# Kernel optimization log

Hardware: AMD Instinct MI355X
Metric: run time of the kernel (lower is better)

## Reference

```python
import jax, jax.numpy as jnp
import numpy as np

B, N, H = 1024, 4096, 32


def setup_inputs() -> dict:
    key = jax.random.key(0)
    ks = jax.random.split(key, 9)
    node_embedding = jax.random.normal(ks[0], (B, N, H), dtype=jnp.float32)
    mask = jax.random.randint(ks[1], (B, N), 0, 2).astype(jnp.float32)
    times = jax.random.uniform(ks[2], (B,), dtype=jnp.float32)
    idxc = jax.random.randint(ks[3], (B, 1), 0, N)
    # parameters
    vf = jax.random.uniform(ks[4], (1, H), dtype=jnp.float32)
    lim1 = 1.0 / np.sqrt(2 * H + 1)
    W1 = jax.random.uniform(ks[5], (H, 2 * H + 1), minval=-lim1, maxval=lim1, dtype=jnp.float32)
    b1 = jax.random.uniform(ks[6], (H,), minval=-lim1, maxval=lim1, dtype=jnp.float32)
    limh = 1.0 / np.sqrt(H)
    Wq = jax.random.uniform(ks[7], (H, H), minval=-limh, maxval=limh, dtype=jnp.float32)
    Wk = jax.random.uniform(ks[8], (H, H), minval=-limh, maxval=limh, dtype=jnp.float32)
    return {"node_embedding": node_embedding, "mask": mask, "times": times,
            "vf": vf, "W1": W1, "b1": b1, "Wq": Wq, "Wk": Wk, "idxc": idxc}


def reference(node_embedding, mask, times, vf, W1, b1, Wq, Wk, idxc):
    h = node_embedding.shape[-1]
    node_avg = jnp.mean(node_embedding, axis=1)                       # [B, H]
    # gather per-batch context node (idxc path; vf used only when idxc is None)
    f = jnp.take_along_axis(node_embedding, idxc[:, :, None], axis=1)[:, 0, :]  # [B, H]
    cat = jnp.concatenate([node_avg, f, times[:, None]], axis=1)      # [B, 2H+1]
    emb = cat @ W1.T + b1                                             # [B, H]
    q = emb @ Wq.T                                                    # [B, H]
    k = node_embedding @ Wk.T                                         # [B, N, H]
    scores = jnp.einsum('bh,bnh->bn', q, k) / jnp.sqrt(jnp.asarray(h, emb.dtype))
    scores = scores - mask * 999999999.0
    return jax.nn.softmax(scores, axis=-1)
```

## Files before the change

### kernel.cpp

```cpp
#include <hip/hip_runtime.h>
#include <math.h>

#define BB 1024
#define NN 4096
#define HH 32
#define PP 4
#define RK1 (NN / PP)

#define WS_PART 0
#define WS_QK   (BB * PP * HH)

__global__ __launch_bounds__(256) void k1_colsum(
    const float* __restrict__ ne, float* __restrict__ ws)
{
    const int blk = blockIdx.x;
    const int b   = blk >> 2;
    const int p   = blk & (PP - 1);
    const int tid = threadIdx.x;
    const int q8  = tid & 7;
    const int r   = tid >> 3;

    __shared__ float s_part[256 * 4];

    const float* base = ne + (size_t)b * (NN * HH)
                           + (size_t)(p * RK1 + r) * HH + q8 * 4;
    float a0 = 0.f, a1 = 0.f, a2 = 0.f, a3 = 0.f;
    #pragma unroll 8
    for (int i = 0; i < RK1 / 32; ++i) {
        const float4 v = *reinterpret_cast<const float4*>(base + i * (32 * HH));
        a0 += v.x; a1 += v.y; a2 += v.z; a3 += v.w;
    }
    *reinterpret_cast<float4*>(&s_part[tid * 4]) = make_float4(a0, a1, a2, a3);
    __syncthreads();

    if (tid < HH) {
        const int q = tid >> 2, j = tid & 3;
        float s = 0.f;
        #pragma unroll
        for (int rr = 0; rr < 32; ++rr) s += s_part[(rr * 8 + q) * 4 + j];
        ws[WS_PART + (b * PP + p) * HH + tid] = s;
    }
}

__global__ __launch_bounds__(64) void k2_mlp(
    const float* __restrict__ ne, const float* __restrict__ times,
    const float* __restrict__ W1, const float* __restrict__ b1,
    const float* __restrict__ Wq, const float* __restrict__ Wk,
    const int* __restrict__ idxc, float* __restrict__ ws)
{
    const int b   = blockIdx.x;
    const int tid = threadIdx.x;
    __shared__ float sh_avg[HH], sh_f[HH], sh_emb[HH], sh_q[HH];

    if (tid < HH) {
        float s = 0.f;
        #pragma unroll
        for (int p = 0; p < PP; ++p) s += ws[WS_PART + (b * PP + p) * HH + tid];
        sh_avg[tid] = s * (1.0f / (float)NN);
        sh_f[tid]   = ne[(size_t)b * (NN * HH) + (size_t)idxc[b] * HH + tid];
    }
    __syncthreads();
    if (tid < HH) {
        const float t = times[b];
        const float* w = W1 + tid * (2 * HH + 1);
        float e = b1[tid];
        #pragma unroll
        for (int j = 0; j < HH; ++j) e += sh_avg[j] * w[j];
        #pragma unroll
        for (int j = 0; j < HH; ++j) e += sh_f[j] * w[HH + j];
        e += t * w[2 * HH];
        sh_emb[tid] = e;
    }
    __syncthreads();
    if (tid < HH) {
        const float* w = Wq + tid * HH;
        float qv = 0.f;
        #pragma unroll
        for (int j = 0; j < HH; ++j) qv += sh_emb[j] * w[j];
        sh_q[tid] = qv;
    }
    __syncthreads();
    if (tid < HH) {
        float s = 0.f;
        #pragma unroll
        for (int h = 0; h < HH; ++h) s += sh_q[h] * Wk[h * HH + tid];
        ws[WS_QK + b * HH + tid] = s * 0.17677669529663687f;
    }
}

__global__ __launch_bounds__(256) void k3_scores(
    const float* __restrict__ ne, const float* __restrict__ mask,
    const float* __restrict__ ws, float* __restrict__ out)
{
    const int b   = blockIdx.x;
    const int tid = threadIdx.x;
    const int q8  = tid & 7;
    const int r   = tid >> 3;

    __shared__ float s_scores[NN];
    __shared__ float sh_qk[HH];
    __shared__ float red_buf[4];

    if (tid < HH) sh_qk[tid] = ws[WS_QK + b * HH + tid];
    __syncthreads();

    const float kq0 = sh_qk[q8 * 4 + 0];
    const float kq1 = sh_qk[q8 * 4 + 1];
    const float kq2 = sh_qk[q8 * 4 + 2];
    const float kq3 = sh_qk[q8 * 4 + 3];

    const float* base = ne + (size_t)b * (NN * HH) + (size_t)r * HH + q8 * 4;

    #pragma unroll 8
    for (int i = 0; i < NN / 32; ++i) {
        const float4 v = *reinterpret_cast<const float4*>(base + i * (32 * HH));
        float p = v.x * kq0 + v.y * kq1 + v.z * kq2 + v.w * kq3;
        p += __shfl_xor(p, 1);
        p += __shfl_xor(p, 2);
        p += __shfl_xor(p, 4);
        if (q8 == 0) s_scores[r + i * 32] = p;
    }
    __syncthreads();

    const float* mrow = mask + (size_t)b * NN;
    float lmax = -INFINITY;
    #pragma unroll
    for (int k = 0; k < NN / 256; ++k) {
        const int n = tid + k * 256;
        const float sc = s_scores[n] - mrow[n] * 999999999.0f;
        s_scores[n] = sc;
        lmax = fmaxf(lmax, sc);
    }
    #pragma unroll
    for (int m = 1; m < 64; m <<= 1) lmax = fmaxf(lmax, __shfl_xor(lmax, m));
    if ((tid & 63) == 0) red_buf[tid >> 6] = lmax;
    __syncthreads();
    const float bmax = fmaxf(fmaxf(red_buf[0], red_buf[1]),
                             fmaxf(red_buf[2], red_buf[3]));

    float lsum = 0.f;
    #pragma unroll
    for (int k = 0; k < NN / 256; ++k) {
        const int n = tid + k * 256;
        const float e = expf(s_scores[n] - bmax);
        s_scores[n] = e;
        lsum += e;
    }
    #pragma unroll
    for (int m = 1; m < 64; m <<= 1) lsum += __shfl_xor(lsum, m);
    __syncthreads();
    if ((tid & 63) == 0) red_buf[tid >> 6] = lsum;
    __syncthreads();
    const float inv = 1.0f / (red_buf[0] + red_buf[1] + red_buf[2] + red_buf[3]);

    float* orow = out + (size_t)b * NN;
    #pragma unroll
    for (int k = 0; k < NN / 256; ++k) {
        const int n = tid + k * 256;
        orow[n] = s_scores[n] * inv;
    }
}

extern "C" void kernel_launch(void* const* d_in, const int* in_sizes, int n_in,
                              void* d_out, int out_size, void* d_ws, size_t ws_size,
                              hipStream_t stream) {
    (void)in_sizes; (void)n_in; (void)ws_size; (void)out_size;
    const float* ne    = (const float*)d_in[0];
    const float* mask  = (const float*)d_in[1];
    const float* times = (const float*)d_in[2];
    const float* W1    = (const float*)d_in[4];
    const float* b1    = (const float*)d_in[5];
    const float* Wq    = (const float*)d_in[6];
    const float* Wk    = (const float*)d_in[7];
    const int*   idxc  = (const int*)d_in[8];
    float* out = (float*)d_out;
    float* ws  = (float*)d_ws;

    k1_colsum<<<dim3(BB * PP), dim3(256), 0, stream>>>(ne, ws);
    k2_mlp<<<dim3(BB), dim3(64), 0, stream>>>(ne, times, W1, b1, Wq, Wk, idxc, ws);
    k3_scores<<<dim3(BB), dim3(256), 0, stream>>>(ne, mask, ws, out);
}
```

Measured before the change: 200.6 us.

## Pipeline column-sum and score stages across batch chunks in one fused kernel

Merges the MLP step into the score kernel and splits the batch into chunks. Each launch runs the column sums for chunk c alongside the MLP and softmax for chunk c-1. Because both stages read the same batch rows close together in time, the second read of node embeddings can hit in the last-level cache instead of HBM. The cost is 9 launches instead of 3, plus a branchy fused kernel that reserves the large shared-memory allocation even in the column-sum blocks, which may lower their occupancy.

Measured after the change: 617.2 us. 208% more time.

```diff
diff --git a/kernel.cpp b/kernel.cpp
--- a/kernel.cpp
+++ b/kernel.cpp
@@ -6,51 +6,71 @@
 #define HH 32
 #define PP 4
 #define RK1 (NN / PP)
+#define CHUNK 128
+#define NCH (BB / CHUNK)
+#define K1B (CHUNK * PP)
+#define K3B CHUNK
 
 #define WS_PART 0
-#define WS_QK   (BB * PP * HH)
 
-__global__ __launch_bounds__(256) void k1_colsum(
-    const float* __restrict__ ne, float* __restrict__ ws)
+__global__ __launch_bounds__(256) void pipe(
+    const float* __restrict__ ne,
+    const float* __restrict__ mask,
+    const float* __restrict__ times,
+    const float* __restrict__ W1,
+    const float* __restrict__ b1,
+    const float* __restrict__ Wq,
+    const float* __restrict__ Wk,
+    const int*   __restrict__ idxc,
+    float* __restrict__ ws,
+    float* __restrict__ out,
+    int k1c, int k3c)
 {
-    const int blk = blockIdx.x;
-    const int b   = blk >> 2;
-    const int p   = blk & (PP - 1);
+    __shared__ float smem[NN + 160];
     const int tid = threadIdx.x;
+
+    if ((int)blockIdx.x < K1B) {
+        if (k1c < 0) return;
+        const int blk = blockIdx.x;
+        const int b   = k1c * CHUNK + (blk >> 2);
+        const int p   = blk & (PP - 1);
+        const int q8  = tid & 7;
+        const int r   = tid >> 3;
+
+        float* s_part = smem;
+
+        const float* base = ne + (size_t)b * (NN * HH)
+                               + (size_t)(p * RK1 + r) * HH + q8 * 4;
+        float a0 = 0.f, a1 = 0.f, a2 = 0.f, a3 = 0.f;
+        #pragma unroll 8
+        for (int i = 0; i < RK1 / 32; ++i) {
+            const float4 v = *reinterpret_cast<const float4*>(base + i * (32 * HH));
+            a0 += v.x; a1 += v.y; a2 += v.z; a3 += v.w;
+        }
+        *reinterpret_cast<float4*>(&s_part[tid * 4]) = make_float4(a0, a1, a2, a3);
+        __syncthreads();
+
+        if (tid < HH) {
+            const int q = tid >> 2, j = tid & 3;
+            float s = 0.f;
+            #pragma unroll
+            for (int rr = 0; rr < 32; ++rr) s += s_part[(rr * 8 + q) * 4 + j];
+            ws[WS_PART + (b * PP + p) * HH + tid] = s;
+        }
+        return;
+    }
+
+    if (k3c < 0) return;
+    const int b   = k3c * CHUNK + ((int)blockIdx.x - K1B);
     const int q8  = tid & 7;
     const int r   = tid >> 3;
 
-    __shared__ float s_part[256 * 4];
-
-    const float* base = ne + (size_t)b * (NN * HH)
-                           + (size_t)(p * RK1 + r) * HH + q8 * 4;
-    float a0 = 0.f, a1 = 0.f, a2 = 0.f, a3 = 0.f;
-    #pragma unroll 8
-    for (int i = 0; i < RK1 / 32; ++i) {
-        const float4 v = *reinterpret_cast<const float4*>(base + i * (32 * HH));
-        a0 += v.x; a1 += v.y; a2 += v.z; a3 += v.w;
-    }
-    *reinterpret_cast<float4*>(&s_part[tid * 4]) = make_float4(a0, a1, a2, a3);
-    __syncthreads();
-
-    if (tid < HH) {
-        const int q = tid >> 2, j = tid & 3;
-        float s = 0.f;
-        #pragma unroll
-        for (int rr = 0; rr < 32; ++rr) s += s_part[(rr * 8 + q) * 4 + j];
-        ws[WS_PART + (b * PP + p) * HH + tid] = s;
-    }
-}
-
-__global__ __launch_bounds__(64) void k2_mlp(
-    const float* __restrict__ ne, const float* __restrict__ times,
-    const float* __restrict__ W1, const float* __restrict__ b1,
-    const float* __restrict__ Wq, const float* __restrict__ Wk,
-    const int* __restrict__ idxc, float* __restrict__ ws)
-{
-    const int b   = blockIdx.x;
-    const int tid = threadIdx.x;
-    __shared__ float sh_avg[HH], sh_f[HH], sh_emb[HH], sh_q[HH];
+    float* s_scores = smem;
+    float* sh_avg   = smem + NN;
+    float* sh_f     = smem + NN + 32;
+    float* sh_emb   = smem + NN + 64;
+    float* sh_qk    = smem + NN + 96;
+    float* red_buf  = smem + NN + 128;
 
     if (tid < HH) {
         float s = 0.f;
@@ -77,31 +97,15 @@
         float qv = 0.f;
         #pragma unroll
         for (int j = 0; j < HH; ++j) qv += sh_emb[j] * w[j];
-        sh_q[tid] = qv;
+        sh_f[tid] = qv;
     }
     __syncthreads();
     if (tid < HH) {
         float s = 0.f;
         #pragma unroll
-        for (int h = 0; h < HH; ++h) s += sh_q[h] * Wk[h * HH + tid];
-        ws[WS_QK + b * HH + tid] = s * 0.17677669529663687f;
+        for (int h = 0; h < HH; ++h) s += sh_f[h] * Wk[h * HH + tid];
+        sh_qk[tid] = s * 0.17677669529663687f;
     }
-}
-
-__global__ __launch_bounds__(256) void k3_scores(
-    const float* __restrict__ ne, const float* __restrict__ mask,
-    const float* __restrict__ ws, float* __restrict__ out)
-{
-    const int b   = blockIdx.x;
-    const int tid = threadIdx.x;
-    const int q8  = tid & 7;
-    const int r   = tid >> 3;
-
-    __shared__ float s_scores[NN];
-    __shared__ float sh_qk[HH];
-    __shared__ float red_buf[4];
-
-    if (tid < HH) sh_qk[tid] = ws[WS_QK + b * HH + tid];
     __syncthreads();
 
     const float kq0 = sh_qk[q8 * 4 + 0];
@@ -176,7 +180,12 @@
     float* out = (float*)d_out;
     float* ws  = (float*)d_ws;
 
-    k1_colsum<<<dim3(BB * PP), dim3(256), 0, stream>>>(ne, ws);
-    k2_mlp<<<dim3(BB), dim3(64), 0, stream>>>(ne, times, W1, b1, Wq, Wk, idxc, ws);
-    k3_scores<<<dim3(BB), dim3(256), 0, stream>>>(ne, mask, ws, out);
+    pipe<<<dim3(K1B), dim3(256), 0, stream>>>(
+        ne, mask, times, W1, b1, Wq, Wk, idxc, ws, out, 0, -1);
+    for (int c = 1; c < NCH; ++c) {
+        pipe<<<dim3(K1B + K3B), dim3(256), 0, stream>>>(
+            ne, mask, times, W1, b1, Wq, Wk, idxc, ws, out, c, c - 1);
+    }
+    pipe<<<dim3(K1B + K3B), dim3(256), 0, stream>>>(
+        ne, mask, times, W1, b1, Wq, Wk, idxc, ws, out, -1, NCH - 1);
 }
```

## Split score/softmax kernel across four row chunks with two-pass rescale

Applied to the files above, without the earlier changes.

The score kernel now runs four blocks per batch row, each computing scores for a quarter of the nodes, a local max and sum, and writing unnormalized exponentials plus per-chunk stats. A new rescale kernel merges the chunk stats online-softmax style and rescales the output in place. This raises block count and parallelism for the bandwidth-heavy pass over node_embedding, but adds an extra read and write of the output and one more launch.

New measurement: 213.2 us. +6.3%, slower.

```diff
diff --git a/kernel.cpp b/kernel.cpp
--- a/kernel.cpp
+++ b/kernel.cpp
@@ -6,9 +6,12 @@
 #define HH 32
 #define PP 4
 #define RK1 (NN / PP)
+#define QQ 4
+#define RQ (NN / QQ)
 
 #define WS_PART 0
 #define WS_QK   (BB * PP * HH)
+#define WS_MS   (WS_QK + BB * HH)
 
 __global__ __launch_bounds__(256) void k1_colsum(
     const float* __restrict__ ne, float* __restrict__ ws)
@@ -88,20 +91,27 @@
     }
 }
 
-__global__ __launch_bounds__(256) void k3_scores(
+__global__ __launch_bounds__(256) void k3a_scores(
     const float* __restrict__ ne, const float* __restrict__ mask,
-    const float* __restrict__ ws, float* __restrict__ out)
-{
-    const int b   = blockIdx.x;
+    const float* __restrict__ ws, float* __restrict__ out,
+    float* __restrict__ ws_ms)
+{
+    const int blk = blockIdx.x;
+    const int b   = blk >> 2;
+    const int q   = blk & (QQ - 1);
     const int tid = threadIdx.x;
     const int q8  = tid & 7;
     const int r   = tid >> 3;
 
-    __shared__ float s_scores[NN];
+    __shared__ float s_scores[RQ];
     __shared__ float sh_qk[HH];
     __shared__ float red_buf[4];
+    __shared__ float red_sum[4];
 
     if (tid < HH) sh_qk[tid] = ws[WS_QK + b * HH + tid];
+
+    const float4 mv = *reinterpret_cast<const float4*>(
+        mask + (size_t)b * NN + q * RQ + tid * 4);
     __syncthreads();
 
     const float kq0 = sh_qk[q8 * 4 + 0];
@@ -109,10 +119,11 @@
     const float kq2 = sh_qk[q8 * 4 + 2];
     const float kq3 = sh_qk[q8 * 4 + 3];
 
-    const float* base = ne + (size_t)b * (NN * HH) + (size_t)r * HH + q8 * 4;
+    const float* base = ne + (size_t)b * (NN * HH)
+                           + (size_t)(q * RQ + r) * HH + q8 * 4;
 
     #pragma unroll 8
-    for (int i = 0; i < NN / 32; ++i) {
+    for (int i = 0; i < RQ / 32; ++i) {
         const float4 v = *reinterpret_cast<const float4*>(base + i * (32 * HH));
         float p = v.x * kq0 + v.y * kq1 + v.z * kq2 + v.w * kq3;
         p += __shfl_xor(p, 1);
@@ -122,15 +133,13 @@
     }
     __syncthreads();
 
-    const float* mrow = mask + (size_t)b * NN;
-    float lmax = -INFINITY;
-    #pragma unroll
-    for (int k = 0; k < NN / 256; ++k) {
-        const int n = tid + k * 256;
-        const float sc = s_scores[n] - mrow[n] * 999999999.0f;
-        s_scores[n] = sc;
-        lmax = fmaxf(lmax, sc);
-    }
+    const float4 s4 = *reinterpret_cast<const float4*>(&s_scores[tid * 4]);
+    float sc0 = s4.x - mv.x * 999999999.0f;
+    float sc1 = s4.y - mv.y * 999999999.0f;
+    float sc2 = s4.z - mv.z * 999999999.0f;
+    float sc3 = s4.w - mv.w * 999999999.0f;
+
+    float lmax = fmaxf(fmaxf(sc0, sc1), fmaxf(sc2, sc3));
     #pragma unroll
     for (int m = 1; m < 64; m <<= 1) lmax = fmaxf(lmax, __shfl_xor(lmax, m));
     if ((tid & 63) == 0) red_buf[tid >> 6] = lmax;
@@ -138,27 +147,49 @@
     const float bmax = fmaxf(fmaxf(red_buf[0], red_buf[1]),
                              fmaxf(red_buf[2], red_buf[3]));
 
-    float lsum = 0.f;
-    #pragma unroll
-    for (int k = 0; k < NN / 256; ++k) {
-        const int n = tid + k * 256;
-        const float e = expf(s_scores[n] - bmax);
-        s_scores[n] = e;
-        lsum += e;
-    }
+    const float e0 = expf(sc0 - bmax);
+    const float e1 = expf(sc1 - bmax);
+    const float e2 = expf(sc2 - bmax);
+    const float e3 = expf(sc3 - bmax);
+    float lsum = (e0 + e1) + (e2 + e3);
     #pragma unroll
     for (int m = 1; m < 64; m <<= 1) lsum += __shfl_xor(lsum, m);
-    __syncthreads();
-    if ((tid & 63) == 0) red_buf[tid >> 6] = lsum;
-    __syncthreads();
-    const float inv = 1.0f / (red_buf[0] + red_buf[1] + red_buf[2] + red_buf[3]);
-
-    float* orow = out + (size_t)b * NN;
-    #pragma unroll
-    for (int k = 0; k < NN / 256; ++k) {
-        const int n = tid + k * 256;
-        orow[n] = s_scores[n] * inv;
-    }
+    if ((tid & 63) == 0) red_sum[tid >> 6] = lsum;
+
+    *reinterpret_cast<float4*>(out + (size_t)b * NN + q * RQ + tid * 4) =
+        make_float4(e0, e1, e2, e3);
+
+    __syncthreads();
+    if (tid == 0) {
+        const float bsum = (red_sum[0] + red_sum[1]) + (red_sum[2] + red_sum[3]);
+        ws_ms[(b * QQ + q) * 2 + 0] = bmax;
+        ws_ms[(b * QQ + q) * 2 + 1] = bsum;
+    }
+}
+
+__global__ __launch_bounds__(256) void k3b_rescale(
+    const float* __restrict__ ws_ms, float* __restrict__ out)
+{
+    const int blk = blockIdx.x;
+    const int b   = blk >> 2;
+    const int q   = blk & (QQ - 1);
+    const int tid = threadIdx.x;
+
+    const float m0 = ws_ms[(b * QQ + 0) * 2 + 0], s0 = ws_ms[(b * QQ + 0) * 2 + 1];
+    const float m1 = ws_ms[(b * QQ + 1) * 2 + 0], s1 = ws_ms[(b * QQ + 1) * 2 + 1];
+    const float m2 = ws_ms[(b * QQ + 2) * 2 + 0], s2 = ws_ms[(b * QQ + 2) * 2 + 1];
+    const float m3 = ws_ms[(b * QQ + 3) * 2 + 0], s3 = ws_ms[(b * QQ + 3) * 2 + 1];
+
+    const float M = fmaxf(fmaxf(m0, m1), fmaxf(m2, m3));
+    const float S = s0 * expf(m0 - M) + s1 * expf(m1 - M)
+                  + s2 * expf(m2 - M) + s3 * expf(m3 - M);
+    const float mq = (q == 0) ? m0 : (q == 1) ? m1 : (q == 2) ? m2 : m3;
+    const float scale = expf(mq - M) / S;
+
+    float* p = out + (size_t)b * NN + q * RQ + tid * 4;
+    const float4 v = *reinterpret_cast<const float4*>(p);
+    *reinterpret_cast<float4*>(p) =
+        make_float4(v.x * scale, v.y * scale, v.z * scale, v.w * scale);
 }
 
 extern "C" void kernel_launch(void* const* d_in, const int* in_sizes, int n_in,
@@ -178,5 +209,6 @@
 
     k1_colsum<<<dim3(BB * PP), dim3(256), 0, stream>>>(ne, ws);
     k2_mlp<<<dim3(BB), dim3(64), 0, stream>>>(ne, times, W1, b1, Wq, Wk, idxc, ws);
-    k3_scores<<<dim3(BB), dim3(256), 0, stream>>>(ne, mask, ws, out);
-}
+    k3a_scores<<<dim3(BB * QQ), dim3(256), 0, stream>>>(ne, mask, ws, out, ws + WS_MS);
+    k3b_rescale<<<dim3(BB * QQ), dim3(256), 0, stream>>>(ws + WS_MS, out);
+}
```
